# Kernel optimization log

Hardware: AMD Instinct MI355X
Metric: run time of the kernel (lower is better)

Reference implementation:

```python
import jax, jax.numpy as jnp
import numpy as np

THRESHOLD = 0.5
NEG_POS_RATIO = 3
ALPHA = 1.0
N_CLASSES = 81
B, P, M = 32, 8732, 16


def cxcy_to_xy(c):
    return jnp.concatenate([c[..., :2] - c[..., 2:] / 2, c[..., :2] + c[..., 2:] / 2], -1)


def xy_to_cxcy(x):
    return jnp.concatenate([(x[..., :2] + x[..., 2:]) / 2, x[..., 2:] - x[..., :2]], -1)


def cxcy_to_gcxgcy(c, p):
    # SSD box encoding with variances 0.1 / 0.2
    return jnp.concatenate([(c[..., :2] - p[..., :2]) / (p[..., 2:] / 10.0),
                            jnp.log(c[..., 2:] / p[..., 2:]) * 5.0], -1)


def box_iou(a, b):
    # a: [M,4], b: [P,4] in xy (xmin,ymin,xmax,ymax)
    lt = jnp.maximum(a[:, None, :2], b[None, :, :2])
    rb = jnp.minimum(a[:, None, 2:], b[None, :, 2:])
    wh = jnp.clip(rb - lt, 0.0)
    inter = wh[..., 0] * wh[..., 1]
    area_a = (a[:, 2] - a[:, 0]) * (a[:, 3] - a[:, 1])
    area_b = (b[:, 2] - b[:, 0]) * (b[:, 3] - b[:, 1])
    return inter / (area_a[:, None] + area_b[None, :] - inter)


def setup_inputs() -> dict:
    key = jax.random.key(0)
    k1, k2, k3, k4, k5, k6, k7 = jax.random.split(key, 7)
    predicted_locs = jax.random.normal(k1, (B, P, 4), dtype=jnp.float32)
    predicted_logits = jax.random.normal(k2, (B, P, N_CLASSES), dtype=jnp.float32)
    # valid gt boxes: centers in (0.2,0.8), sizes in (0.05,0.4) -> xy
    cxy = jax.random.uniform(k3, (B, M, 2), minval=0.2, maxval=0.8)
    wh = jax.random.uniform(k4, (B, M, 2), minval=0.05, maxval=0.4)
    boxes = cxcy_to_xy(jnp.concatenate([cxy, wh], -1)).astype(jnp.float32)
    labels = jax.random.randint(k5, (B, M), 1, N_CLASSES)  # real objects: labels >= 1
    # priors: centers in (0,1), positive sizes
    pcxy = jax.random.uniform(k6, (P, 2), minval=0.0, maxval=1.0)
    pwh = jax.random.uniform(k7, (P, 2), minval=0.05, maxval=0.6)
    priors_cxcy = jnp.concatenate([pcxy, pwh], -1).astype(jnp.float32)
    return {"predicted_locs": predicted_locs, "predicted_logits": predicted_logits,
            "boxes": boxes, "labels": labels, "priors_cxcy": priors_cxcy}


def reference(predicted_locs, predicted_logits, boxes, labels, priors_cxcy):
    priors_xy = cxcy_to_xy(priors_cxcy)

    def match(bx, lb):  # bx: [M,4] xy, lb: [M] int
        overlap = box_iou(bx, priors_xy)                # [M, P]
        overlap_for_each_prior = overlap.max(axis=0)    # [P]
        object_for_each_prior = overlap.argmax(axis=0)  # [P]
        prior_for_each_object = overlap.argmax(axis=1)  # [M]
        # force each gt object to be matched to its best prior
        object_for_each_prior = object_for_each_prior.at[prior_for_each_object].set(jnp.arange(M))
        overlap_for_each_prior = overlap_for_each_prior.at[prior_for_each_object].set(1.0)
        label_for_each_prior = lb[object_for_each_prior]
        label_for_each_prior = jnp.where(overlap_for_each_prior < THRESHOLD, 0, label_for_each_prior)
        true_locs = cxcy_to_gcxgcy(xy_to_cxcy(bx[object_for_each_prior]), priors_cxcy)
        return true_locs, label_for_each_prior

    true_locs, true_classes = jax.vmap(match)(boxes, labels)  # [B,P,4], [B,P]

    positive = true_classes != 0                 # [B,P]
    n_positives = positive.sum(axis=1)           # [B]
    n_pos_total = n_positives.sum().astype(jnp.float32)

    # localization: L1Loss (mean) over positive priors only -> mean over 4*n_pos elements
    loc_loss = jnp.sum(jnp.abs(predicted_locs - true_locs) * positive[..., None]) / (4.0 * n_pos_total)

    # per-prior cross entropy, nan/inf -> 0 as in the original
    logp = jax.nn.log_softmax(predicted_logits, axis=-1)
    conf_loss_all = -jnp.take_along_axis(logp, true_classes[..., None], axis=-1)[..., 0]  # [B,P]
    conf_loss_all = jnp.nan_to_num(conf_loss_all, nan=0.0, posinf=0.0, neginf=0.0)

    conf_loss_pos_sum = jnp.sum(conf_loss_all * positive)
    conf_loss_neg = jnp.where(positive, 0.0, conf_loss_all)
    conf_loss_neg = -jnp.sort(-conf_loss_neg, axis=1)  # descending sort per image
    ranks = jnp.arange(P)[None, :]
    hard_negatives = ranks < (NEG_POS_RATIO * n_positives)[:, None]
    conf_loss_hard_neg_sum = jnp.sum(conf_loss_neg * hard_negatives)

    conf_loss = (conf_loss_hard_neg_sum + conf_loss_pos_sum) / n_pos_total
    return conf_loss + ALPHA * loc_loss
```

## Files before the change

kernel.cpp:

```cpp
#include <hip/hip_runtime.h>
#include <math.h>

#define BB 32
#define PP 8732
#define MM 16
#define NC 81
#define THRESH 0.5f
#define NPR 3
#define CHUNKS 16
#define CHUNK ((PP + CHUNKS - 1) / CHUNKS)
#define SBLK 64

__global__ void __launch_bounds__(256) match_part_kernel(
    const float* __restrict__ boxes,
    const float* __restrict__ priors,
    unsigned long long* __restrict__ keys_part,
    unsigned* __restrict__ done)
{
    const int b = blockIdx.x / CHUNKS;
    const int c = blockIdx.x % CHUNKS;
    const int tid = threadIdx.x;
    if (blockIdx.x == 0 && tid == 0) *done = 0u;

    __shared__ float s_box[MM][4];
    __shared__ float s_area[MM];
    __shared__ float s_bv[4 * MM];
    __shared__ int   s_bi[4 * MM];

    if (tid < MM * 4) ((float*)s_box)[tid] = boxes[b * MM * 4 + tid];
    __syncthreads();
    if (tid < MM)
        s_area[tid] = (s_box[tid][2] - s_box[tid][0]) * (s_box[tid][3] - s_box[tid][1]);
    __syncthreads();

    float bestv[MM];
    int   bestp[MM];
#pragma unroll
    for (int m = 0; m < MM; ++m) { bestv[m] = -1.0f; bestp[m] = 0; }

    const int p0 = c * CHUNK;
    const int p1 = (p0 + CHUNK < PP) ? (p0 + CHUNK) : PP;
    for (int p = p0 + tid; p < p1; p += 256) {
        const float4 pr = ((const float4*)priors)[p];
        float px0 = pr.x - pr.z * 0.5f, py0 = pr.y - pr.w * 0.5f;
        float px1 = pr.x + pr.z * 0.5f, py1 = pr.y + pr.w * 0.5f;
        float parea = (px1 - px0) * (py1 - py0);
#pragma unroll
        for (int m = 0; m < MM; ++m) {
            float lx = fmaxf(s_box[m][0], px0);
            float ly = fmaxf(s_box[m][1], py0);
            float rx = fminf(s_box[m][2], px1);
            float ry = fminf(s_box[m][3], py1);
            float w = fmaxf(rx - lx, 0.0f);
            float h = fmaxf(ry - ly, 0.0f);
            float inter = w * h;
            float iou = inter / (s_area[m] + parea - inter);
            if (iou > bestv[m]) { bestv[m] = iou; bestp[m] = p; }
        }
    }

    const int lane = tid & 63, wid = tid >> 6;
#pragma unroll
    for (int m = 0; m < MM; ++m) {
        float v = bestv[m]; int i = bestp[m];
        for (int off = 32; off > 0; off >>= 1) {
            float ov = __shfl_xor(v, off);
            int   oi = __shfl_xor(i, off);
            if (ov > v || (ov == v && oi < i)) { v = ov; i = oi; }
        }
        if (lane == 0) { s_bv[wid * MM + m] = v; s_bi[wid * MM + m] = i; }
    }
    __syncthreads();

    if (tid == 0) {
        for (int m = 0; m < MM; ++m) {
            float v = s_bv[m]; int i = s_bi[m];
            for (int w = 1; w < 4; ++w) {
                float ov = s_bv[w * MM + m]; int oi = s_bi[w * MM + m];
                if (ov > v || (ov == v && oi < i)) { v = ov; i = oi; }
            }
            if (v < 0.0f) v = 0.0f;
            keys_part[(b * CHUNKS + c) * MM + m] =
                ((unsigned long long)__float_as_uint(v) << 32) |
                (unsigned long long)(0x7FFFFFFFu - (unsigned)i);
        }
    }
}

__global__ void __launch_bounds__(256) conf_kernel(
    const float* __restrict__ logits,
    const float* __restrict__ plocs,
    const float* __restrict__ boxes,
    const int*   __restrict__ labels,
    const float* __restrict__ priors,
    const unsigned long long* __restrict__ keys_part,
    float* __restrict__ neg,
    int*   __restrict__ cnt_part,
    float* __restrict__ conf_part,
    float* __restrict__ loc_part)
{
    const int tid = threadIdx.x;
    const int lane = tid & 63;
    const int g = lane >> 4;
    const int i = lane & 15;
    const int b = blockIdx.x / SBLK;
    const int s = blockIdx.x % SBLK;

    __shared__ float s_box[MM][4];
    __shared__ float s_area[MM];
    __shared__ int   s_lab[MM];
    __shared__ int   s_fp[MM];
    __shared__ unsigned long long s_keys[CHUNKS * MM];

    if (tid < MM * 4) ((float*)s_box)[tid] = boxes[b * MM * 4 + tid];
    if (tid < MM) s_lab[tid] = labels[b * MM + tid];
    s_keys[tid] = keys_part[b * CHUNKS * MM + tid];
    __syncthreads();
    if (tid < MM) {
        s_area[tid] = (s_box[tid][2] - s_box[tid][0]) * (s_box[tid][3] - s_box[tid][1]);
        unsigned long long best = 0ull;
#pragma unroll
        for (int c = 0; c < CHUNKS; ++c) {
            unsigned long long k = s_keys[c * MM + tid];
            if (k > best) best = k;
        }
        s_fp[tid] = (int)(0x7FFFFFFFu - (unsigned)(best & 0xFFFFFFFFull));
    }
    __syncthreads();

    const float bxx0 = s_box[i][0], bxy0 = s_box[i][1];
    const float bxx1 = s_box[i][2], bxy1 = s_box[i][3];
    const float barea = s_area[i];
    const int   myfp  = s_fp[i];

    const int w0 = s * 4 + (tid >> 6);
    const int GPI = PP / 4;

    int   pcnt = 0;
    float pconf = 0.0f, ploc = 0.0f;

    for (int wi = w0; wi < GPI; wi += SBLK * 4) {
        const int rp = wi * 4 + g;
        const int r = b * PP + rp;

        const float4 pr = ((const float4*)priors)[rp];
        float px0 = pr.x - pr.z * 0.5f, py0 = pr.y - pr.w * 0.5f;
        float px1 = pr.x + pr.z * 0.5f, py1 = pr.y + pr.w * 0.5f;
        float parea = (px1 - px0) * (py1 - py0);
        float lx = fmaxf(bxx0, px0), ly = fmaxf(bxy0, py0);
        float rx = fminf(bxx1, px1), ry = fminf(bxy1, py1);
        float inter = fmaxf(rx - lx, 0.0f) * fmaxf(ry - ly, 0.0f);
        float ov = inter / (barea + parea - inter);
        int bm = i;
#pragma unroll
        for (int off = 8; off > 0; off >>= 1) {
            float o2 = __shfl_xor(ov, off);
            int   i2 = __shfl_xor(bm, off);
            if (o2 > ov || (o2 == ov && i2 < bm)) { ov = o2; bm = i2; }
        }
        unsigned long long bal = __ballot(myfp == rp);
        unsigned gm = (unsigned)((bal >> (g * 16)) & 0xFFFFull);
        int o, cls;
        if (gm) { o = 31 - __clz(gm); cls = s_lab[o]; }
        else    { o = bm; cls = (ov < THRESH) ? 0 : s_lab[bm]; }

        const size_t base = (size_t)r * NC;
        float e0 = logits[base + i];
        float e1 = logits[base + 16 + i];
        float e2 = logits[base + 32 + i];
        float e3 = logits[base + 48 + i];
        float e4 = logits[base + 64 + i];
        float e5 = (i == 0) ? logits[base + 80] : -INFINITY;

        float mx = fmaxf(fmaxf(fmaxf(e0, e1), fmaxf(e2, e3)), fmaxf(e4, e5));
#pragma unroll
        for (int off = 8; off > 0; off >>= 1) mx = fmaxf(mx, __shfl_xor(mx, off));
        float sum = __expf(e0 - mx) + __expf(e1 - mx) + __expf(e2 - mx) +
                    __expf(e3 - mx) + __expf(e4 - mx) +
                    ((i == 0) ? __expf(e5 - mx) : 0.0f);
#pragma unroll
        for (int off = 8; off > 0; off >>= 1) sum += __shfl_xor(sum, off);

        const int k = cls >> 4, ci = cls & 15;
        float ek = (k == 0) ? e0 : (k == 1) ? e1 : (k == 2) ? e2 :
                   (k == 3) ? e3 : (k == 4) ? e4 : e5;
        float xc = __shfl(ek, (g << 4) + ci);
        float conf = mx + __logf(sum) - xc;
        if (!isfinite(conf)) conf = 0.0f;

        if (i == 0) {
            neg[r] = (cls == 0) ? conf : 0.0f;
            if (cls != 0) {
                pcnt += 1;
                pconf += conf;
                float cx = (s_box[o][0] + s_box[o][2]) * 0.5f;
                float cy = (s_box[o][1] + s_box[o][3]) * 0.5f;
                float w4 = s_box[o][2] - s_box[o][0];
                float h4 = s_box[o][3] - s_box[o][1];
                float g0 = (cx - pr.x) / (pr.z / 10.0f);
                float g1 = (cy - pr.y) / (pr.w / 10.0f);
                float g2 = logf(w4 / pr.z) * 5.0f;
                float g3 = logf(h4 / pr.w) * 5.0f;
                const float4 pl = ((const float4*)plocs)[r];
                ploc += fabsf(pl.x - g0) + fabsf(pl.y - g1) +
                        fabsf(pl.z - g2) + fabsf(pl.w - g3);
            }
        }
    }

    __shared__ int   s4i[4];
    __shared__ float s4c[4], s4l[4];
#pragma unroll
    for (int off = 32; off > 0; off >>= 1) {
        pcnt  += __shfl_xor(pcnt, off);
        pconf += __shfl_xor(pconf, off);
        ploc  += __shfl_xor(ploc, off);
    }
    const int wv = tid >> 6;
    if (lane == 0) { s4i[wv] = pcnt; s4c[wv] = pconf; s4l[wv] = ploc; }
    __syncthreads();
    if (tid == 0) {
        cnt_part[blockIdx.x]  = s4i[0] + s4i[1] + s4i[2] + s4i[3];
        conf_part[blockIdx.x] = s4c[0] + s4c[1] + s4c[2] + s4c[3];
        loc_part[blockIdx.x]  = s4l[0] + s4l[1] + s4l[2] + s4l[3];
    }
}

#define TPK 1024
#define VPT ((PP + TPK - 1) / TPK)

__global__ void __launch_bounds__(TPK) topk_final_kernel(
    const float* __restrict__ neg, const int* __restrict__ cnt_part,
    const float* __restrict__ conf_part, const float* __restrict__ loc_part,
    float* __restrict__ hardneg, unsigned* __restrict__ done,
    float* __restrict__ out)
{
    const int b = blockIdx.x;
    const int tid = threadIdx.x;
    const int lane = tid & 63, wid = tid >> 6;
    __shared__ int s16i[16];
    __shared__ float s16f[16];
    __shared__ int s_k;
    __shared__ int s_last;

    if (tid < 64) {
        int c = cnt_part[b * SBLK + tid];
#pragma unroll
        for (int off = 32; off > 0; off >>= 1) c += __shfl_xor(c, off);
        if (tid == 0) s_k = NPR * c;
    }

    unsigned v[VPT];
#pragma unroll
    for (int j = 0; j < VPT; ++j) {
        int p = tid + j * TPK;
        v[j] = (p < PP) ? __float_as_uint(neg[b * PP + p]) : 0u;
    }
    __syncthreads();

    int K = s_k;
    if (K > PP) K = PP;
    if (K > 0) {
        unsigned lo = 0u, hi = 0x7fffffffu;
        while (lo < hi) {
            unsigned mid = lo + ((hi - lo + 1u) >> 1);
            int cnt = 0;
#pragma unroll
            for (int j = 0; j < VPT; ++j) cnt += (v[j] >= mid);
#pragma unroll
            for (int off = 32; off > 0; off >>= 1) cnt += __shfl_xor(cnt, off);
            if (lane == 0) s16i[wid] = cnt;
            __syncthreads();
            int total = 0;
#pragma unroll
            for (int j = 0; j < 16; ++j) total += s16i[j];
            __syncthreads();
            if (total >= K) lo = mid; else hi = mid - 1u;
        }
        const unsigned kth = lo;

        int cgt = 0; float sgt = 0.0f;
#pragma unroll
        for (int j = 0; j < VPT; ++j) {
            if (v[j] > kth) { cgt++; sgt += __uint_as_float(v[j]); }
        }
#pragma unroll
        for (int off = 32; off > 0; off >>= 1) {
            cgt += __shfl_xor(cgt, off);
            sgt += __shfl_xor(sgt, off);
        }
        if (lane == 0) { s16i[wid] = cgt; s16f[wid] = sgt; }
        __syncthreads();
        if (tid == 0) {
            int cgt_t = 0; float sum_gt = 0.0f;
#pragma unroll
            for (int j = 0; j < 16; ++j) { cgt_t += s16i[j]; sum_gt += s16f[j]; }
            hardneg[b] = sum_gt + (float)(K - cgt_t) * __uint_as_float(kth);
        }
    } else {
        if (tid == 0) hardneg[b] = 0.0f;
    }

    __threadfence();
    if (tid == 0) {
        unsigned old = atomicAdd(done, 1u);
        s_last = (old == BB - 1) ? 1 : 0;
    }
    __syncthreads();
    if (!s_last) return;
    __threadfence();

    int np = 0; float cf = 0.0f, lc = 0.0f, hn = 0.0f;
    for (int j = tid; j < BB * SBLK; j += TPK) {
        np += cnt_part[j];
        cf += conf_part[j];
        lc += loc_part[j];
    }
    if (tid < BB) hn = hardneg[tid];
#pragma unroll
    for (int off = 32; off > 0; off >>= 1) {
        np += __shfl_xor(np, off);
        cf += __shfl_xor(cf, off);
        lc += __shfl_xor(lc, off);
        hn += __shfl_xor(hn, off);
    }
    if (lane == 0) { s16i[wid] = np; s16f[wid] = cf; }
    __shared__ float s16l[16], s16h[16];
    if (lane == 0) { s16l[wid] = lc; s16h[wid] = hn; }
    __syncthreads();
    if (tid == 0) {
        int npt_i = 0; float cft = 0.0f, lct = 0.0f, hnt = 0.0f;
#pragma unroll
        for (int j = 0; j < 16; ++j) {
            npt_i += s16i[j]; cft += s16f[j]; lct += s16l[j]; hnt += s16h[j];
        }
        float npt = (float)npt_i;
        out[0] = (hnt + cft) / npt + lct / (4.0f * npt);
    }
}

extern "C" void kernel_launch(void* const* d_in, const int* in_sizes, int n_in,
                              void* d_out, int out_size, void* d_ws, size_t ws_size,
                              hipStream_t stream) {
    (void)in_sizes; (void)n_in; (void)out_size; (void)ws_size;
    const float* plocs  = (const float*)d_in[0];
    const float* logits = (const float*)d_in[1];
    const float* boxes  = (const float*)d_in[2];
    const int*   labels = (const int*)d_in[3];
    const float* priors = (const float*)d_in[4];
    float* out = (float*)d_out;

    char* ws = (char*)d_ws;
    float* neg      = (float*)ws; ws += (size_t)BB * PP * 4;
    unsigned long long* keys_part = (unsigned long long*)ws; ws += (size_t)BB * CHUNKS * MM * 8;
    int*   cnt_part  = (int*)ws;   ws += BB * SBLK * 4;
    float* conf_part = (float*)ws; ws += BB * SBLK * 4;
    float* loc_part  = (float*)ws; ws += BB * SBLK * 4;
    float* hardneg   = (float*)ws; ws += BB * 4;
    unsigned* done   = (unsigned*)ws; ws += 4;


    match_part_kernel<<<BB * CHUNKS, 256, 0, stream>>>(boxes, priors, keys_part, done);

    conf_kernel<<<BB * SBLK, 256, 0, stream>>>(logits, plocs, boxes, labels, priors,
                                               keys_part, neg,
                                               cnt_part, conf_part, loc_part);

    topk_final_kernel<<<BB, TPK, 0, stream>>>(neg, cnt_part, conf_part, loc_part,
                                              hardneg, done, out);
}
```

Baseline: 87.43 us.

## Store per-prior best overlap in match pass and use 4-ary radix select

The match kernel now records each prior's best IoU and object index into workspace arrays, so the conf kernel reads them instead of recomputing IoU against all boxes with shuffle reductions. The per-image top-k threshold search moves from a 31-step binary search to a 4-ary search that tests three thresholds per round, halving the number of block-wide reduction and barrier rounds. The cost is extra global writes and reads of two B*P arrays, plus packed 16-bit counters that assume each count stays below 65536.

Result: faster. 81.15 us (-7.2%).

```diff
diff --git a/kernel.cpp b/kernel.cpp
--- a/kernel.cpp
+++ b/kernel.cpp
@@ -14,6 +14,8 @@
 __global__ void __launch_bounds__(256) match_part_kernel(
     const float* __restrict__ boxes,
     const float* __restrict__ priors,
+    float* __restrict__ ovl,
+    int* __restrict__ obj,
     unsigned long long* __restrict__ keys_part,
     unsigned* __restrict__ done)
 {
@@ -45,6 +47,7 @@
         float px0 = pr.x - pr.z * 0.5f, py0 = pr.y - pr.w * 0.5f;
         float px1 = pr.x + pr.z * 0.5f, py1 = pr.y + pr.w * 0.5f;
         float parea = (px1 - px0) * (py1 - py0);
+        float bv = -1.0f; int bm = 0;
 #pragma unroll
         for (int m = 0; m < MM; ++m) {
             float lx = fmaxf(s_box[m][0], px0);
@@ -55,8 +58,11 @@
             float h = fmaxf(ry - ly, 0.0f);
             float inter = w * h;
             float iou = inter / (s_area[m] + parea - inter);
+            if (iou > bv) { bv = iou; bm = m; }
             if (iou > bestv[m]) { bestv[m] = iou; bestp[m] = p; }
         }
+        ovl[b * PP + p] = bv;
+        obj[b * PP + p] = bm;
     }
 
     const int lane = tid & 63, wid = tid >> 6;
@@ -93,6 +99,8 @@
     const float* __restrict__ boxes,
     const int*   __restrict__ labels,
     const float* __restrict__ priors,
+    const float* __restrict__ ovl,
+    const int*   __restrict__ obj,
     const unsigned long long* __restrict__ keys_part,
     float* __restrict__ neg,
     int*   __restrict__ cnt_part,
@@ -107,7 +115,6 @@
     const int s = blockIdx.x % SBLK;
 
     __shared__ float s_box[MM][4];
-    __shared__ float s_area[MM];
     __shared__ int   s_lab[MM];
     __shared__ int   s_fp[MM];
     __shared__ unsigned long long s_keys[CHUNKS * MM];
@@ -117,7 +124,6 @@
     s_keys[tid] = keys_part[b * CHUNKS * MM + tid];
     __syncthreads();
     if (tid < MM) {
-        s_area[tid] = (s_box[tid][2] - s_box[tid][0]) * (s_box[tid][3] - s_box[tid][1]);
         unsigned long long best = 0ull;
 #pragma unroll
         for (int c = 0; c < CHUNKS; ++c) {
@@ -128,10 +134,7 @@
     }
     __syncthreads();
 
-    const float bxx0 = s_box[i][0], bxy0 = s_box[i][1];
-    const float bxx1 = s_box[i][2], bxy1 = s_box[i][3];
-    const float barea = s_area[i];
-    const int   myfp  = s_fp[i];
+    const int myfp = s_fp[i];
 
     const int w0 = s * 4 + (tid >> 6);
     const int GPI = PP / 4;
@@ -142,27 +145,14 @@
     for (int wi = w0; wi < GPI; wi += SBLK * 4) {
         const int rp = wi * 4 + g;
         const int r = b * PP + rp;
-
-        const float4 pr = ((const float4*)priors)[rp];
-        float px0 = pr.x - pr.z * 0.5f, py0 = pr.y - pr.w * 0.5f;
-        float px1 = pr.x + pr.z * 0.5f, py1 = pr.y + pr.w * 0.5f;
-        float parea = (px1 - px0) * (py1 - py0);
-        float lx = fmaxf(bxx0, px0), ly = fmaxf(bxy0, py0);
-        float rx = fminf(bxx1, px1), ry = fminf(bxy1, py1);
-        float inter = fmaxf(rx - lx, 0.0f) * fmaxf(ry - ly, 0.0f);
-        float ov = inter / (barea + parea - inter);
-        int bm = i;
-#pragma unroll
-        for (int off = 8; off > 0; off >>= 1) {
-            float o2 = __shfl_xor(ov, off);
-            int   i2 = __shfl_xor(bm, off);
-            if (o2 > ov || (o2 == ov && i2 < bm)) { ov = o2; bm = i2; }
-        }
+        const float ov = ovl[r];
+        const int om = obj[r];
+
         unsigned long long bal = __ballot(myfp == rp);
         unsigned gm = (unsigned)((bal >> (g * 16)) & 0xFFFFull);
         int o, cls;
         if (gm) { o = 31 - __clz(gm); cls = s_lab[o]; }
-        else    { o = bm; cls = (ov < THRESH) ? 0 : s_lab[bm]; }
+        else    { o = om; cls = (ov < THRESH) ? 0 : s_lab[om]; }
 
         const size_t base = (size_t)r * NC;
         float e0 = logits[base + i];
@@ -193,6 +183,7 @@
             if (cls != 0) {
                 pcnt += 1;
                 pconf += conf;
+                const float4 pr = ((const float4*)priors)[rp];
                 float cx = (s_box[o][0] + s_box[o][2]) * 0.5f;
                 float cy = (s_box[o][1] + s_box[o][3]) * 0.5f;
                 float w4 = s_box[o][2] - s_box[o][0];
@@ -238,7 +229,7 @@
     const int b = blockIdx.x;
     const int tid = threadIdx.x;
     const int lane = tid & 63, wid = tid >> 6;
-    __shared__ int s16i[16];
+    __shared__ int s16a[16], s16b[16];
     __shared__ float s16f[16];
     __shared__ int s_k;
     __shared__ int s_last;
@@ -261,21 +252,47 @@
     int K = s_k;
     if (K > PP) K = PP;
     if (K > 0) {
-        unsigned lo = 0u, hi = 0x7fffffffu;
-        while (lo < hi) {
-            unsigned mid = lo + ((hi - lo + 1u) >> 1);
-            int cnt = 0;
-#pragma unroll
-            for (int j = 0; j < VPT; ++j) cnt += (v[j] >= mid);
-#pragma unroll
-            for (int off = 32; off > 0; off >>= 1) cnt += __shfl_xor(cnt, off);
-            if (lane == 0) s16i[wid] = cnt;
+        unsigned lo = 0u;
+        {
+            const unsigned m1 = 0x40000000u;
+            int c1 = 0;
+#pragma unroll
+            for (int j = 0; j < VPT; ++j) c1 += (v[j] >= m1);
+#pragma unroll
+            for (int off = 32; off > 0; off >>= 1) c1 += __shfl_xor(c1, off);
+            if (lane == 0) s16a[wid] = c1;
             __syncthreads();
-            int total = 0;
-#pragma unroll
-            for (int j = 0; j < 16; ++j) total += s16i[j];
+            int n1 = 0;
+#pragma unroll
+            for (int j = 0; j < 16; ++j) n1 += s16a[j];
             __syncthreads();
-            if (total >= K) lo = mid; else hi = mid - 1u;
+            if (n1 >= K) lo = m1;
+        }
+        unsigned span = 0x40000000u;
+        for (int it = 0; it < 15; ++it) {
+            span >>= 2;
+            const unsigned m1 = lo + span;
+            const unsigned m2 = lo + 2 * span;
+            const unsigned m3 = lo + 3 * span;
+            int c12 = 0, c3 = 0;
+#pragma unroll
+            for (int j = 0; j < VPT; ++j) {
+                c12 += (v[j] >= m1) + ((int)(v[j] >= m2) << 16);
+                c3  += (v[j] >= m3);
+            }
+#pragma unroll
+            for (int off = 32; off > 0; off >>= 1) {
+                c12 += __shfl_xor(c12, off);
+                c3  += __shfl_xor(c3, off);
+            }
+            if (lane == 0) { s16a[wid] = c12; s16b[wid] = c3; }
+            __syncthreads();
+            int t12 = 0, t3 = 0;
+#pragma unroll
+            for (int j = 0; j < 16; ++j) { t12 += s16a[j]; t3 += s16b[j]; }
+            __syncthreads();
+            const int n1 = t12 & 0xFFFF, n2 = t12 >> 16, n3 = t3;
+            lo = (n3 >= K) ? m3 : (n2 >= K) ? m2 : (n1 >= K) ? m1 : lo;
         }
         const unsigned kth = lo;
 
@@ -289,12 +306,12 @@
             cgt += __shfl_xor(cgt, off);
             sgt += __shfl_xor(sgt, off);
         }
-        if (lane == 0) { s16i[wid] = cgt; s16f[wid] = sgt; }
+        if (lane == 0) { s16a[wid] = cgt; s16f[wid] = sgt; }
         __syncthreads();
         if (tid == 0) {
             int cgt_t = 0; float sum_gt = 0.0f;
 #pragma unroll
-            for (int j = 0; j < 16; ++j) { cgt_t += s16i[j]; sum_gt += s16f[j]; }
+            for (int j = 0; j < 16; ++j) { cgt_t += s16a[j]; sum_gt += s16f[j]; }
             hardneg[b] = sum_gt + (float)(K - cgt_t) * __uint_as_float(kth);
         }
     } else {
@@ -324,15 +341,14 @@
         lc += __shfl_xor(lc, off);
         hn += __shfl_xor(hn, off);
     }
-    if (lane == 0) { s16i[wid] = np; s16f[wid] = cf; }
     __shared__ float s16l[16], s16h[16];
-    if (lane == 0) { s16l[wid] = lc; s16h[wid] = hn; }
+    if (lane == 0) { s16a[wid] = np; s16f[wid] = cf; s16l[wid] = lc; s16h[wid] = hn; }
     __syncthreads();
     if (tid == 0) {
         int npt_i = 0; float cft = 0.0f, lct = 0.0f, hnt = 0.0f;
 #pragma unroll
         for (int j = 0; j < 16; ++j) {
-            npt_i += s16i[j]; cft += s16f[j]; lct += s16l[j]; hnt += s16h[j];
+            npt_i += s16a[j]; cft += s16f[j]; lct += s16l[j]; hnt += s16h[j];
         }
         float npt = (float)npt_i;
         out[0] = (hnt + cft) / npt + lct / (4.0f * npt);
@@ -351,6 +367,8 @@
     float* out = (float*)d_out;
 
     char* ws = (char*)d_ws;
+    float* ovl      = (float*)ws; ws += (size_t)BB * PP * 4;
+    int*   obj      = (int*)ws;   ws += (size_t)BB * PP * 4;
     float* neg      = (float*)ws; ws += (size_t)BB * PP * 4;
     unsigned long long* keys_part = (unsigned long long*)ws; ws += (size_t)BB * CHUNKS * MM * 8;
     int*   cnt_part  = (int*)ws;   ws += BB * SBLK * 4;
@@ -360,10 +378,11 @@
     unsigned* done   = (unsigned*)ws; ws += 4;
 
 
-    match_part_kernel<<<BB * CHUNKS, 256, 0, stream>>>(boxes, priors, keys_part, done);
+    match_part_kernel<<<BB * CHUNKS, 256, 0, stream>>>(boxes, priors, ovl, obj,
+                                                       keys_part, done);
 
     conf_kernel<<<BB * SBLK, 256, 0, stream>>>(logits, plocs, boxes, labels, priors,
-                                               keys_part, neg,
+                                               ovl, obj, keys_part, neg,
                                                cnt_part, conf_part, loc_part);
 
     topk_final_kernel<<<BB, TPK, 0, stream>>>(neg, cnt_part, conf_part, loc_part,
```
